# Optimization experiments

Measured on AMD Instinct MI355X. Metric: run time of the kernel, lower is better.

Reference implementation:

```python
import jax, jax.numpy as jnp
import numpy as np

B, C, H, W = 8, 256, 56, 56
R = 2
E = C // R  # embed_dim = in_channels // r


def setup_inputs() -> dict:
    key = jax.random.key(0)
    ks = jax.random.split(key, 10)
    s = 0.02
    return {
        "x": jax.random.normal(ks[0], (B, C, H, W), jnp.float32),
        "Wq": jax.random.normal(ks[1], (E, C), jnp.float32) * s,
        "bq": jax.random.normal(ks[2], (E,), jnp.float32) * s,
        "Wk": jax.random.normal(ks[3], (E, C), jnp.float32) * s,
        "bk": jax.random.normal(ks[4], (E,), jnp.float32) * s,
        "Wv": jax.random.normal(ks[5], (E, C), jnp.float32) * s,
        "bv": jax.random.normal(ks[6], (E,), jnp.float32) * s,
        "Wcat": jax.random.normal(ks[7], (1, 2 * E), jnp.float32) * s,  # 1x1 conv, no bias
        "Wexp": jax.random.normal(ks[8], (C, E), jnp.float32) * s,
        "bexp": jax.random.normal(ks[9], (C,), jnp.float32) * s,
    }


def reference(x, Wq, bq, Wk, bk, Wv, bv, Wcat, Wexp, bexp):
    b, c, h, w = x.shape
    n = h * w
    xf = x.reshape(b, c, n)  # 1x1 convs are channel matmuls over flattened pixels
    q = jnp.einsum('ec,bcn->ben', Wq, xf) + bq[None, :, None]   # [b,E,n]
    k = jnp.einsum('ec,bcn->ben', Wk, xf) + bk[None, :, None]   # [b,E,n]
    v = jnp.einsum('ec,bcn->bne', Wv, xf) + bv[None, None, :]   # [b,n,E]
    # concat_project 1x1 conv on qk=[q;k] repeated along a new n2 axis.
    # NOTE: source repeats BOTH q and k as 'b c n1 -> b c n1 n2', so the score
    # is constant along n2: s[b,n1] = ReLU(wq.q[:,n1] + wk.k[:,n1]).
    wq_c, wk_c = Wcat[0, :E], Wcat[0, E:]
    s = jax.nn.relu(jnp.einsum('e,ben->bn', wq_c, q)
                    + jnp.einsum('e,ben->bn', wk_c, k))         # [b,n]
    attn = jnp.broadcast_to(s[:, :, None], (b, n, n)) / n       # [b,n,n]
    embed = jnp.einsum('bij,bje->bie', attn, v)                 # [b,n,E]
    out = jnp.einsum('ce,bne->bcn', Wexp, embed) + bexp[None, :, None]
    return out.reshape(b, c, h, w) + x
```

## Files before the change

kernel.cpp:

```cpp
#include <hip/hip_runtime.h>

#define CC 256
#define EE 128
#define BB 8
#define NN 3136
#define NN4 784
#define TILES 13

__device__ __forceinline__ float waveReduceSum(float v) {
    #pragma unroll
    for (int off = 32; off > 0; off >>= 1) v += __shfl_down(v, off, 64);
    return v;
}

__global__ void k_xbar(const float* __restrict__ x, float* __restrict__ xbar) {
    int row = blockIdx.x;
    int tid = threadIdx.x;
    const float4* xr = (const float4*)(x + (size_t)row * NN);
    float acc = 0.f;
    for (int i = tid; i < NN4; i += 256) {
        float4 v = xr[i];
        acc += (v.x + v.y) + (v.z + v.w);
    }
    acc = waveReduceSum(acc);
    __shared__ float red[4];
    int wid = tid >> 6, lane = tid & 63;
    if (lane == 0) red[wid] = acc;
    __syncthreads();
    if (tid == 0) xbar[row] = (red[0] + red[1] + red[2] + red[3]) * (1.0f / NN);
}

__global__ void k_small(const float* __restrict__ xbar,
                        const float* __restrict__ Wq, const float* __restrict__ bq,
                        const float* __restrict__ Wk, const float* __restrict__ bk,
                        const float* __restrict__ Wv, const float* __restrict__ bv,
                        const float* __restrict__ Wcat,
                        const float* __restrict__ Wexp, const float* __restrict__ bexp,
                        float* __restrict__ gb, float* __restrict__ Aout,
                        float* __restrict__ cst) {
    int b = blockIdx.x, tid = threadIdx.x;
    __shared__ float xb_s[CC];
    __shared__ float vb_s[EE];
    xb_s[tid] = xbar[b * CC + tid];
    __syncthreads();
    if (tid < EE) {
        float acc = bv[tid];
        const float* wr = Wv + tid * CC;
        #pragma unroll 8
        for (int c = 0; c < CC; c++) acc += wr[c] * xb_s[c];
        vb_s[tid] = acc;
    }
    __syncthreads();
    {
        float acc = 0.f;
        const float* we = Wexp + tid * EE;
        #pragma unroll 8
        for (int e = 0; e < EE; e++) acc += we[e] * vb_s[e];
        gb[b * CC + tid] = acc + bexp[tid];
    }
    if (b == 0) {
        float a = 0.f;
        #pragma unroll 4
        for (int e = 0; e < EE; e++)
            a += Wcat[e] * Wq[e * CC + tid] + Wcat[EE + e] * Wk[e * CC + tid];
        Aout[tid] = a;
        if (tid == 0) {
            float s = 0.f;
            for (int e = 0; e < EE; e++)
                s += Wcat[e] * bq[e] + Wcat[EE + e] * bk[e];
            cst[0] = s;
        }
    }
}

__global__ void k_s(const float* __restrict__ x, const float* __restrict__ A,
                    const float* __restrict__ cst, float* __restrict__ s_out) {
    __shared__ float A_s[CC];
    int tid = threadIdx.x;
    A_s[tid] = A[tid];
    __syncthreads();
    int b = blockIdx.x / TILES;
    int it = blockIdx.x - b * TILES;
    int i = it * 256 + tid;
    if (i < NN) {
        const float* xb = x + (size_t)b * CC * NN + i;
        float acc = 0.f;
        #pragma unroll 8
        for (int c = 0; c < CC; c++) acc += A_s[c] * xb[(size_t)c * NN];
        float v = acc + cst[0];
        s_out[b * NN + i] = fmaxf(v, 0.f);
    }
}

__global__ void k_out(const float* __restrict__ x, const float* __restrict__ s,
                      const float* __restrict__ gb, float* __restrict__ out) {
    int idx = blockIdx.x * 256 + threadIdx.x;
    int row = idx / NN4;
    int i4 = idx - row * NN4;
    int b = row >> 8;
    float g = gb[row];
    float4 xv = ((const float4*)x)[idx];
    float4 sv = ((const float4*)(s + (size_t)b * NN))[i4];
    float4 o;
    o.x = fmaf(sv.x, g, xv.x);
    o.y = fmaf(sv.y, g, xv.y);
    o.z = fmaf(sv.z, g, xv.z);
    o.w = fmaf(sv.w, g, xv.w);
    ((float4*)out)[idx] = o;
}

extern "C" void kernel_launch(void* const* d_in, const int* in_sizes, int n_in,
                              void* d_out, int out_size, void* d_ws, size_t ws_size,
                              hipStream_t stream) {
    const float* x    = (const float*)d_in[0];
    const float* Wq   = (const float*)d_in[1];
    const float* bq   = (const float*)d_in[2];
    const float* Wk   = (const float*)d_in[3];
    const float* bk   = (const float*)d_in[4];
    const float* Wv   = (const float*)d_in[5];
    const float* bv   = (const float*)d_in[6];
    const float* Wcat = (const float*)d_in[7];
    const float* Wexp = (const float*)d_in[8];
    const float* bexp = (const float*)d_in[9];
    float* out = (float*)d_out;

    float* ws   = (float*)d_ws;
    float* xbar = ws;
    float* gb   = ws + 2048;
    float* A    = ws + 4096;
    float* cst  = ws + 4352;
    float* s    = ws + 4368;

    k_xbar<<<BB * CC, 256, 0, stream>>>(x, xbar);
    k_small<<<BB, 256, 0, stream>>>(xbar, Wq, bq, Wk, bk, Wv, bv, Wcat, Wexp, bexp,
                                    gb, A, cst);
    k_s<<<BB * TILES, 256, 0, stream>>>(x, A, cst, s);
    k_out<<<(BB * CC * NN4) / 256, 256, 0, stream>>>(x, s, gb, out);
}
```

Baseline: 137.5 us.

## Fuse score and output kernels into one tiled pass over x

Merges the per-pixel score kernel and the elementwise output kernel into one kernel. Each block handles 64 pixels across all 256 channels: it computes the score with a split-channel reduction in shared memory, then writes the output from the same tile, so the score buffer is no longer written and read through global memory. The small kernel is also rewritten to use wave-cooperative dot products with coalesced weight reads. The fused kernel runs only 392 blocks and reads x twice per block, which lowers parallelism compared with the large separate elementwise kernel.

```diff
diff --git a/kernel.cpp b/kernel.cpp
--- a/kernel.cpp
+++ b/kernel.cpp
@@ -5,7 +5,8 @@
 #define BB 8
 #define NN 3136
 #define NN4 784
-#define TILES 13
+#define T4 16
+#define NTILES 49
 
 __device__ __forceinline__ float waveReduceSum(float v) {
     #pragma unroll
@@ -35,78 +36,116 @@
                         const float* __restrict__ Wk, const float* __restrict__ bk,
                         const float* __restrict__ Wv, const float* __restrict__ bv,
                         const float* __restrict__ Wcat,
-                        const float* __restrict__ Wexp, const float* __restrict__ bexp,
-                        float* __restrict__ gb, float* __restrict__ Aout,
+                        const float* __restrict__ Wexp,
+                        float* __restrict__ gexp, float* __restrict__ Aout,
                         float* __restrict__ cst) {
     int b = blockIdx.x, tid = threadIdx.x;
+    int w = tid >> 6, lane = tid & 63;
     __shared__ float xb_s[CC];
     __shared__ float vb_s[EE];
     xb_s[tid] = xbar[b * CC + tid];
     __syncthreads();
-    if (tid < EE) {
-        float acc = bv[tid];
-        const float* wr = Wv + tid * CC;
-        #pragma unroll 8
-        for (int c = 0; c < CC; c++) acc += wr[c] * xb_s[c];
-        vb_s[tid] = acc;
+    for (int r = 0; r < 32; r++) {
+        int e = w * 32 + r;
+        const float* wr = Wv + e * CC;
+        float acc = wr[lane]        * xb_s[lane]
+                  + wr[64 + lane]   * xb_s[64 + lane]
+                  + wr[128 + lane]  * xb_s[128 + lane]
+                  + wr[192 + lane]  * xb_s[192 + lane];
+        acc = waveReduceSum(acc);
+        if (lane == 0) vb_s[e] = acc + bv[e];
     }
     __syncthreads();
-    {
-        float acc = 0.f;
-        const float* we = Wexp + tid * EE;
-        #pragma unroll 8
-        for (int e = 0; e < EE; e++) acc += we[e] * vb_s[e];
-        gb[b * CC + tid] = acc + bexp[tid];
+    for (int r = 0; r < 64; r++) {
+        int c = w * 64 + r;
+        const float* we = Wexp + c * EE;
+        float acc = we[lane] * vb_s[lane] + we[64 + lane] * vb_s[64 + lane];
+        acc = waveReduceSum(acc);
+        if (lane == 0) gexp[b * CC + c] = acc;
     }
     if (b == 0) {
         float a = 0.f;
-        #pragma unroll 4
+        #pragma unroll 8
         for (int e = 0; e < EE; e++)
             a += Wcat[e] * Wq[e * CC + tid] + Wcat[EE + e] * Wk[e * CC + tid];
         Aout[tid] = a;
-        if (tid == 0) {
-            float s = 0.f;
-            for (int e = 0; e < EE; e++)
-                s += Wcat[e] * bq[e] + Wcat[EE + e] * bk[e];
-            cst[0] = s;
+        if (tid < 64) {
+            float cp = Wcat[tid] * bq[tid] + Wcat[tid + 64] * bq[tid + 64]
+                     + Wcat[EE + tid] * bk[tid] + Wcat[EE + tid + 64] * bk[tid + 64];
+            cp = waveReduceSum(cp);
+            if (tid == 0) cst[0] = cp;
         }
     }
 }
 
-__global__ void k_s(const float* __restrict__ x, const float* __restrict__ A,
-                    const float* __restrict__ cst, float* __restrict__ s_out) {
+__global__ void __launch_bounds__(256) k_fused(
+        const float* __restrict__ x, const float* __restrict__ A,
+        const float* __restrict__ cst, const float* __restrict__ gexp,
+        const float* __restrict__ bexp, float* __restrict__ out) {
+    int b = blockIdx.x / NTILES;
+    int tile = blockIdx.x - b * NTILES;
+    int tid = threadIdx.x;
+    int i4l = tid & 15, cg = tid >> 4;
+
     __shared__ float A_s[CC];
-    int tid = threadIdx.x;
-    A_s[tid] = A[tid];
+    __shared__ float g_s[CC];
+    __shared__ float be_s[CC];
+    __shared__ float4 part[16][16];
+    __shared__ float4 s_s[16];
+
+    A_s[tid]  = A[tid];
+    g_s[tid]  = gexp[b * CC + tid];
+    be_s[tid] = bexp[tid];
     __syncthreads();
-    int b = blockIdx.x / TILES;
-    int it = blockIdx.x - b * TILES;
-    int i = it * 256 + tid;
-    if (i < NN) {
-        const float* xb = x + (size_t)b * CC * NN + i;
-        float acc = 0.f;
-        #pragma unroll 8
-        for (int c = 0; c < CC; c++) acc += A_s[c] * xb[(size_t)c * NN];
-        float v = acc + cst[0];
-        s_out[b * NN + i] = fmaxf(v, 0.f);
+
+    const float4* x4 = (const float4*)x + (size_t)b * CC * NN4 + tile * T4;
+    float4*       o4 = (float4*)out     + (size_t)b * CC * NN4 + tile * T4;
+
+    float4 acc = make_float4(0.f, 0.f, 0.f, 0.f);
+    #pragma unroll
+    for (int j = 0; j < 16; j++) {
+        int c = cg * 16 + j;
+        float a = A_s[c];
+        float4 v = x4[(size_t)c * NN4 + i4l];
+        acc.x = fmaf(a, v.x, acc.x);
+        acc.y = fmaf(a, v.y, acc.y);
+        acc.z = fmaf(a, v.z, acc.z);
+        acc.w = fmaf(a, v.w, acc.w);
     }
-}
+    part[cg][i4l] = acc;
+    __syncthreads();
+    if (tid < 16) {
+        float4 sum = part[0][tid];
+        #pragma unroll
+        for (int g = 1; g < 16; g++) {
+            float4 p = part[g][tid];
+            sum.x += p.x; sum.y += p.y; sum.z += p.z; sum.w += p.w;
+        }
+        float cv = cst[0];
+        float4 s;
+        s.x = fmaxf(sum.x + cv, 0.f);
+        s.y = fmaxf(sum.y + cv, 0.f);
+        s.z = fmaxf(sum.z + cv, 0.f);
+        s.w = fmaxf(sum.w + cv, 0.f);
+        s_s[tid] = s;
+    }
+    __syncthreads();
 
-__global__ void k_out(const float* __restrict__ x, const float* __restrict__ s,
-                      const float* __restrict__ gb, float* __restrict__ out) {
-    int idx = blockIdx.x * 256 + threadIdx.x;
-    int row = idx / NN4;
-    int i4 = idx - row * NN4;
-    int b = row >> 8;
-    float g = gb[row];
-    float4 xv = ((const float4*)x)[idx];
-    float4 sv = ((const float4*)(s + (size_t)b * NN))[i4];
-    float4 o;
-    o.x = fmaf(sv.x, g, xv.x);
-    o.y = fmaf(sv.y, g, xv.y);
-    o.z = fmaf(sv.z, g, xv.z);
-    o.w = fmaf(sv.w, g, xv.w);
-    ((float4*)out)[idx] = o;
+    float4 sv = s_s[i4l];
+    #pragma unroll
+    for (int j = 0; j < 16; j++) {
+        int c = j * 16 + cg;
+        float g  = g_s[c];
+        float be = be_s[c];
+        size_t off = (size_t)c * NN4 + i4l;
+        float4 xv = x4[off];
+        float4 o;
+        o.x = fmaf(sv.x, g, xv.x) + be;
+        o.y = fmaf(sv.y, g, xv.y) + be;
+        o.z = fmaf(sv.z, g, xv.z) + be;
+        o.w = fmaf(sv.w, g, xv.w) + be;
+        o4[off] = o;
+    }
 }
 
 extern "C" void kernel_launch(void* const* d_in, const int* in_sizes, int n_in,
@@ -126,14 +165,12 @@
 
     float* ws   = (float*)d_ws;
     float* xbar = ws;
-    float* gb   = ws + 2048;
+    float* gexp = ws + 2048;
     float* A    = ws + 4096;
     float* cst  = ws + 4352;
-    float* s    = ws + 4368;
 
     k_xbar<<<BB * CC, 256, 0, stream>>>(x, xbar);
-    k_small<<<BB, 256, 0, stream>>>(xbar, Wq, bq, Wk, bk, Wv, bv, Wcat, Wexp, bexp,
-                                    gb, A, cst);
-    k_s<<<BB * TILES, 256, 0, stream>>>(x, A, cst, s);
-    k_out<<<(BB * CC * NN4) / 256, 256, 0, stream>>>(x, s, gb, out);
+    k_small<<<BB, 256, 0, stream>>>(xbar, Wq, bq, Wk, bk, Wv, bv, Wcat, Wexp,
+                                    gexp, A, cst);
+    k_fused<<<BB * NTILES, 256, 0, stream>>>(x, A, cst, gexp, bexp, out);
 }
```

After: 152.8 us. +11.1%, slower.
